# Kernel optimization log

Hardware: AMD Instinct MI355X
Metric: run time of the kernel (lower is better)

The kernel has to match this reference:

```python
import jax, jax.numpy as jnp
import numpy as np

B, CIN, H, W = 4, 128, 128, 128
CH = CIN // 2          # channels after transpose conv (= 64)
COUT = 64
N2 = (B * 2 * H * 2 * W) // 2  # active sites of x2 (half of fine grid)


def setup_inputs() -> dict:
    key = jax.random.key(0)
    ks = jax.random.split(key, 8)
    n = lambda k, s, sc=1.0: jax.random.normal(k, s, jnp.float32) * sc
    return {
        "x1": n(ks[0], (B, CIN, H, W)),
        "x2_feat": n(ks[1], (N2, CH)),
        "w_up": n(ks[2], (CIN, CH, 2, 2), 0.05),   # torch ConvTranspose2d layout [in, out, kh, kw]
        "b_up": n(ks[3], (CH,), 0.05),
        "w1": n(ks[4], (CH, CH, 3, 3), 0.05),      # torch Conv2d layout [out, in, kh, kw]
        "b1": n(ks[5], (CH,), 0.05),
        "a1": jnp.full((1,), 0.25, jnp.float32),   # nn.PReLU default init
        "w2": n(ks[6], (COUT, CH, 3, 3), 0.05),
        "b2": n(ks[7], (COUT,), 0.05),
        "a2": jnp.full((1,), 0.25, jnp.float32),
    }


def _prelu(x, a):
    return jnp.where(x >= 0, x, a * x)


def _conv3(x, w, b):
    y = jax.lax.conv_general_dilated(x, w, (1, 1), 'SAME',
                                     dimension_numbers=('NCHW', 'OIHW', 'NCHW'))
    return y + b[None, :, None, None]


def reference(x1, x2_feat, w_up, b_up, w1, b1, a1, w2, b2, a2):
    Bn, _, Hn, Wn = x1.shape
    # ConvTranspose2d k=2, s=2 (non-overlapping) as an einsum:
    # up[b,o,2i+p,2j+q] = sum_c x1[b,c,i,j] * w_up[c,o,p,q]
    up = jnp.einsum('bchw,copq->bohpwq', x1, w_up).reshape(Bn, CH, 2 * Hn, 2 * Wn)
    up = up + b_up[None, :, None, None]
    # addspvec: larger tensor keeps its indices; first len(b) feature rows
    # are overwritten by the smaller tensor's features (spconv raster order).
    f = jnp.transpose(up, (0, 2, 3, 1)).reshape(-1, CH)  # [B*2H*2W, CH]
    f = f.at[:x2_feat.shape[0]].set(x2_feat)
    merged = jnp.transpose(f.reshape(Bn, 2 * Hn, 2 * Wn, CH), (0, 3, 1, 2))
    # DoubleConv: (SparseConv2d 3x3 pad1 -> PReLU) x 2 (dense-equivalent)
    h = _prelu(_conv3(merged, w1, b1), a1[0])
    out = _prelu(_conv3(h, w2, b2), a2[0])
    return out
```

## Files before the change

kernel.cpp:

```cpp
#include <hip/hip_runtime.h>

typedef __attribute__((ext_vector_type(8))) short short8;
typedef __attribute__((ext_vector_type(4))) float f32x4;

#define HF 256
#define WF 256

typedef const __attribute__((address_space(1))) void gbl_void;
typedef __attribute__((address_space(3))) void lds_void;

__device__ __forceinline__ ushort f2bf(float f) {
    uint u = __builtin_bit_cast(uint, f);
    u = (u + 0x7FFFu + ((u >> 16) & 1u)) >> 16;
    return (ushort)u;
}
__device__ __forceinline__ uint pack2(float a, float b) {
    return (uint)f2bf(a) | ((uint)f2bf(b) << 16);
}
__device__ __forceinline__ float prelu(float v, float al) { return v >= 0.f ? v : al * v; }

__global__ __launch_bounds__(256) void k_wprep(const float* __restrict__ w1,
                                               const float* __restrict__ w2,
                                               const float* __restrict__ wup,
                                               ushort* __restrict__ wT1,
                                               ushort* __restrict__ wT2,
                                               ushort* __restrict__ wupT,
                                               uint4* __restrict__ zeroBuf) {
    int idx = blockIdx.x * 256 + threadIdx.x;
    if (blockIdx.x == 0 && threadIdx.x < 16)
        zeroBuf[threadIdx.x] = make_uint4(0u, 0u, 0u, 0u);
    if (idx < 36864) {
        int tap = idx >> 12;
        int oc  = idx & 4095;
        int src = oc * 9 + tap;
        wT1[idx] = f2bf(w1[src]);
        wT2[idx] = f2bf(w2[src]);
    }
    if (idx < 32768) {
        int out = idx >> 7;
        int c   = idx & 127;
        int k   = out >> 6;
        int o   = out & 63;
        wupT[idx] = f2bf(wup[c * 256 + o * 4 + k]);
    }
}

__global__ __launch_bounds__(512) void k_upsample_mfma(const float* __restrict__ x1,
                                                       const ushort* __restrict__ wupT,
                                                       const float* __restrict__ bup,
                                                       ushort* __restrict__ upB) {
    __shared__ __align__(16) char lds[81920];

    const int t   = threadIdx.x;
    const int l   = t & 63;
    const int l15 = l & 15;
    const int l4  = l >> 4;
    const int w   = t >> 6;
    const int pg  = w & 3;
    const int oh  = w >> 2;
    const int i   = blockIdx.x >> 1;
    const int j0  = (blockIdx.x & 1) * 64;
    const int z   = blockIdx.y;
    const int gb  = 2 + z;

    {
        const int j  = t & 63;
        const int cg = t >> 6;
        const size_t base = ((size_t)gb * 128) * 16384 + (size_t)i * 128 + j0 + j;
        float xv[16];
#pragma unroll
        for (int r = 0; r < 2; ++r)
#pragma unroll
            for (int cc = 0; cc < 8; ++cc)
                xv[r * 8 + cc] = x1[base + (size_t)(cg * 16 + r * 8 + cc) * 16384];
#pragma unroll
        for (int r = 0; r < 2; ++r) {
            short8 pk;
#pragma unroll
            for (int cc = 0; cc < 8; ++cc) pk[cc] = (short)f2bf(xv[r * 8 + cc]);
            int ad = (j * 256 + (cg * 16 + r * 8) * 2) ^ ((j & 15) << 4);
            *(short8*)(lds + ad) = pk;
        }
    }
    {
        const uint4* src = (const uint4*)wupT;
#pragma unroll
        for (int rep = 0; rep < 8; ++rep) {
            int q   = rep * 512 + t;
            int out = q >> 4, c16 = q & 15;
            int ad  = 16384 + ((out * 256 + c16 * 16) ^ ((out & 15) << 4));
            *(uint4*)(lds + ad) = src[q];
        }
    }
    float bvv[4];
#pragma unroll
    for (int ob = 0; ob < 4; ++ob) bvv[ob] = bup[ob * 16 + l15];
    __syncthreads();

    f32x4 acc[2][4];
#pragma unroll
    for (int kk = 0; kk < 2; ++kk)
#pragma unroll
        for (int ob = 0; ob < 4; ++ob) acc[kk][ob] = (f32x4){0.f, 0.f, 0.f, 0.f};

#pragma unroll
    for (int ks = 0; ks < 4; ++ks) {
        const int cb = ks * 64 + (l4 << 4);
        const int rowA = pg * 16 + l15;
        short8 xfr = *(const short8*)(lds + ((rowA * 256 + cb) ^ ((rowA & 15) << 4)));
#pragma unroll
        for (int kk = 0; kk < 2; ++kk)
#pragma unroll
            for (int ob = 0; ob < 4; ++ob) {
                int out = (oh * 2 + kk) * 64 + ob * 16 + l15;
                short8 wfr = *(const short8*)(lds + 16384 +
                              ((out * 256 + cb) ^ ((out & 15) << 4)));
                acc[kk][ob] = __builtin_amdgcn_mfma_f32_16x16x32_bf16(xfr, wfr, acc[kk][ob], 0, 0, 0);
            }
    }
    __syncthreads();

    ushort* OUT = (ushort*)lds;
#pragma unroll
    for (int kk = 0; kk < 2; ++kk) {
        const int k = oh * 2 + kk, p = k >> 1, q = k & 1;
#pragma unroll
        for (int ob = 0; ob < 4; ++ob) {
            const int o = ob * 16 + l15;
#pragma unroll
            for (int r = 0; r < 4; ++r) {
                int jl = pg * 16 + l4 * 4 + r;
                int x  = 2 * jl + q;
                OUT[(p * 128 + x) * 64 + o] = f2bf(acc[kk][ob][r] + bvv[ob]);
            }
        }
    }
    __syncthreads();

#pragma unroll
    for (int rep = 0; rep < 4; ++rep) {
        int idx = rep * 512 + t;
        int p   = idx >> 10;
        int y   = 2 * i + p;
        uint4 v = *(const uint4*)(lds + idx * 16);
        size_t g = (size_t)(z * HF + y) * 2048 + (size_t)j0 * 16 + (idx & 1023);
        ((uint4*)upB)[g] = v;
    }
}

template<int IN_MODE, int OUT_NHWC>
__global__ __launch_bounds__(1024, 1) void k_conv(const float* __restrict__ x2,
                                                  const ushort* __restrict__ upB,
                                                  const ushort* __restrict__ inB,
                                                  const ushort* __restrict__ wT,
                                                  const float* __restrict__ bias,
                                                  const float* __restrict__ alpha,
                                                  const uint4* __restrict__ zeroBuf,
                                                  ushort* __restrict__ outB,
                                                  float* __restrict__ outF) {
    __shared__ __align__(16) ushort inL[5120 * 8];
    __shared__ __align__(16) ushort wL[9 * 64 * 64];

    const int t   = threadIdx.x;
    const int wv  = t >> 6;
    const int l   = t & 63;
    const int l15 = l & 15;
    const int l4  = l >> 4;
    const int x0  = (blockIdx.x & 7) * 32;
    const int y0  = (blockIdx.x >> 3) * 16;
    const int b   = blockIdx.y;

    {
        const char* wTb = (const char*)wT;
#pragma unroll
        for (int rep = 0; rep < 4; ++rep) {
            int d   = rep * 1024 + t;
            int tap = d >> 9;
            int dp  = d & 511;
            int s   = (tap << 9) + (dp ^ ((dp >> 3) & 7));
            __builtin_amdgcn_global_load_lds(
                (gbl_void*)(wTb + (size_t)s * 16),
                (lds_void*)((char*)wL + (size_t)((rep << 10) + (wv << 6)) * 16),
                16, 0, 0);
        }
        if (wv < 8) {
            int d   = 4096 + (wv << 6) + l;
            int tap = d >> 9;
            int dp  = d & 511;
            int s   = (tap << 9) + (dp ^ ((dp >> 3) & 7));
            __builtin_amdgcn_global_load_lds(
                (gbl_void*)(wTb + (size_t)s * 16),
                (lds_void*)((char*)wL + (size_t)(4096 + (wv << 6)) * 16),
                16, 0, 0);
        }
    }

    if (IN_MODE == 1 || b >= 2) {
        const ushort* src0 = (IN_MODE == 1) ? inB : upB;
        const int bb = (IN_MODE == 1) ? b : (b - 2);
#pragma unroll
        for (int rep = 0; rep < 5; ++rep) {
            int d  = rep * 1024 + t;
            int r  = d / 272;
            int wi = d - r * 272;
            int wq = wi ^ ((wi >> 3) & 7);
            int x  = wq >> 3, c8 = wq & 7;
            int gy = y0 - 1 + r;
            int gx = x0 - 1 + x;
            const void* g;
            if (d < 4896 && (unsigned)gy < HF && (unsigned)gx < WF) {
                size_t pos = (size_t)(bb * HF + gy) * WF + gx;
                g = (const void*)(src0 + pos * 64 + c8 * 8);
            } else {
                g = (const void*)zeroBuf;
            }
            __builtin_amdgcn_global_load_lds(
                (gbl_void*)g,
                (lds_void*)((char*)inL + (size_t)((rep << 10) + (wv << 6)) * 16),
                16, 0, 0);
        }
    } else {
        for (int q = t; q < 18 * 34 * 8; q += 1024) {
            int r   = q / 272;
            int rem = q - r * 272;
            int x   = rem >> 3;
            int c8  = rem & 7;
            int gy = y0 - 1 + r;
            int gx = x0 - 1 + x;
            uint4 v = make_uint4(0u, 0u, 0u, 0u);
            if ((unsigned)gy < HF && (unsigned)gx < WF) {
                size_t pos = (size_t)(b * HF + gy) * WF + gx;
                const float4* s = (const float4*)(x2 + pos * 64 + c8 * 8);
                float4 u0 = s[0], u1 = s[1];
                v = make_uint4(pack2(u0.x, u0.y), pack2(u0.z, u0.w),
                               pack2(u1.x, u1.y), pack2(u1.z, u1.w));
            }
            int ad = (q * 16) ^ ((x & 7) << 4);
            *(uint4*)((char*)inL + ad) = v;
        }
    }
    __syncthreads();

    f32x4 acc[2][4];
#pragma unroll
    for (int m = 0; m < 2; ++m)
#pragma unroll
        for (int nf = 0; nf < 4; ++nf) acc[m][nf] = (f32x4){0.f, 0.f, 0.f, 0.f};

#pragma unroll
    for (int tap = 0; tap < 9; ++tap) {
        const int ky = tap / 3;
        const int kx = tap % 3;
        const char* wPage = (const char*)wL + tap * 8192;
#pragma unroll
        for (int ks = 0; ks < 2; ++ks) {
            short8 wfr[4];
#pragma unroll
            for (int nf = 0; nf < 4; ++nf) {
                int o = nf * 16 + l15;
                int ad = (o * 128 + ks * 64 + (l4 << 4)) ^ ((o & 7) << 4);
                wfr[nf] = *(const short8*)(wPage + ad);
            }
#pragma unroll
            for (int m = 0; m < 2; ++m) {
                int ry = wv + ky;
                int xl = m * 16 + l15 + kx;
                int ad = ((ry * 34 + xl) * 128 + ks * 64 + (l4 << 4)) ^ ((xl & 7) << 4);
                short8 ifr = *(const short8*)((const char*)inL + ad);
#pragma unroll
                for (int nf = 0; nf < 4; ++nf) {
                    if (OUT_NHWC)
                        acc[m][nf] = __builtin_amdgcn_mfma_f32_16x16x32_bf16(
                            wfr[nf], ifr, acc[m][nf], 0, 0, 0);
                    else
                        acc[m][nf] = __builtin_amdgcn_mfma_f32_16x16x32_bf16(
                            ifr, wfr[nf], acc[m][nf], 0, 0, 0);
                }
            }
        }
    }

    const float al = alpha[0];
    const int y = y0 + wv;
    if (OUT_NHWC) {
        float4 bv[4];
#pragma unroll
        for (int nf = 0; nf < 4; ++nf) bv[nf] = *(const float4*)(bias + nf * 16 + (l4 << 2));
#pragma unroll
        for (int m = 0; m < 2; ++m) {
            int x = x0 + m * 16 + l15;
#pragma unroll
            for (int nf = 0; nf < 4; ++nf) {
                f32x4 v = acc[m][nf];
                uint lo = pack2(prelu(v.x + bv[nf].x, al), prelu(v.y + bv[nf].y, al));
                uint hi = pack2(prelu(v.z + bv[nf].z, al), prelu(v.w + bv[nf].w, al));
                int cb = nf * 16 + (l4 << 2);
                *(uint2*)(outB + ((size_t)(b * HF + y) * WF + x) * 64 + cb) = make_uint2(lo, hi);
            }
        }
    } else {
        float bb[4];
#pragma unroll
        for (int nf = 0; nf < 4; ++nf) bb[nf] = bias[nf * 16 + l15];
#pragma unroll
        for (int m = 0; m < 2; ++m) {
            int xb = x0 + m * 16 + (l4 << 2);
#pragma unroll
            for (int nf = 0; nf < 4; ++nf) {
                f32x4 v = acc[m][nf];
                int cout = nf * 16 + l15;
                float4 st;
                st.x = prelu(v.x + bb[nf], al);
                st.y = prelu(v.y + bb[nf], al);
                st.z = prelu(v.z + bb[nf], al);
                st.w = prelu(v.w + bb[nf], al);
                *(float4*)(outF + (((size_t)b * 64 + cout) << 16) + y * WF + xb) = st;
            }
        }
    }
}

extern "C" void kernel_launch(void* const* d_in, const int* in_sizes, int n_in,
                              void* d_out, int out_size, void* d_ws, size_t ws_size,
                              hipStream_t stream) {
    const float* x1  = (const float*)d_in[0];
    const float* x2  = (const float*)d_in[1];
    const float* wup = (const float*)d_in[2];
    const float* bup = (const float*)d_in[3];
    const float* w1  = (const float*)d_in[4];
    const float* b1  = (const float*)d_in[5];
    const float* a1  = (const float*)d_in[6];
    const float* w2  = (const float*)d_in[7];
    const float* b2  = (const float*)d_in[8];
    const float* a2  = (const float*)d_in[9];

    char* ws = (char*)d_ws;
    ushort* upB  = (ushort*)ws;
    ushort* hB   = (ushort*)(ws + (size_t)(16 << 20));
    ushort* wT1  = (ushort*)(ws + (size_t)(48 << 20));
    ushort* wT2  = wT1 + 9 * 64 * 64;
    ushort* wupT = wT2 + 9 * 64 * 64;
    uint4*  zeroBuf = (uint4*)(ws + (size_t)(49 << 20));
    float* out = (float*)d_out;

    k_wprep<<<144, 256, 0, stream>>>(w1, w2, wup, wT1, wT2, wupT, zeroBuf);
    k_upsample_mfma<<<dim3(256, 2), 512, 0, stream>>>(x1, wupT, bup, upB);
    k_conv<0, 1><<<dim3(128, 4), 1024, 0, stream>>>(x2, upB, nullptr, wT1, b1, a1, zeroBuf, hB, nullptr);
    k_conv<1, 0><<<dim3(128, 4), 1024, 0, stream>>>(nullptr, nullptr, hB, wT2, b2, a2, zeroBuf, nullptr, out);
}
```

Measured before the change: 80.78 us.

## Halve conv tile height and stream weights in tap chunks for two blocks/CU

```diff
diff --git a/kernel.cpp b/kernel.cpp
--- a/kernel.cpp
+++ b/kernel.cpp
@@ -149,17 +149,17 @@
 }
 
 template<int IN_MODE, int OUT_NHWC>
-__global__ __launch_bounds__(1024, 1) void k_conv(const float* __restrict__ x2,
-                                                  const ushort* __restrict__ upB,
-                                                  const ushort* __restrict__ inB,
-                                                  const ushort* __restrict__ wT,
-                                                  const float* __restrict__ bias,
-                                                  const float* __restrict__ alpha,
-                                                  const uint4* __restrict__ zeroBuf,
-                                                  ushort* __restrict__ outB,
-                                                  float* __restrict__ outF) {
-    __shared__ __align__(16) ushort inL[5120 * 8];
-    __shared__ __align__(16) ushort wL[9 * 64 * 64];
+__global__ __launch_bounds__(512, 2) void k_conv(const float* __restrict__ x2,
+                                                 const ushort* __restrict__ upB,
+                                                 const ushort* __restrict__ inB,
+                                                 const ushort* __restrict__ wT,
+                                                 const float* __restrict__ bias,
+                                                 const float* __restrict__ alpha,
+                                                 const uint4* __restrict__ zeroBuf,
+                                                 ushort* __restrict__ outB,
+                                                 float* __restrict__ outF) {
+    __shared__ __align__(16) ushort inL[2816 * 8];
+    __shared__ __align__(16) ushort wL[4 * 64 * 64];
 
     const int t   = threadIdx.x;
     const int wv  = t >> 6;
@@ -167,60 +167,54 @@
     const int l15 = l & 15;
     const int l4  = l >> 4;
     const int x0  = (blockIdx.x & 7) * 32;
-    const int y0  = (blockIdx.x >> 3) * 16;
+    const int y0  = (blockIdx.x >> 3) * 8;
     const int b   = blockIdx.y;
 
-    {
-        const char* wTb = (const char*)wT;
-#pragma unroll
-        for (int rep = 0; rep < 4; ++rep) {
-            int d   = rep * 1024 + t;
-            int tap = d >> 9;
+    const char* wTb = (const char*)wT;
+
+    auto stage_w = [&](int s) {
+        const int nrep = (s == 2) ? 1 : 4;
+        for (int rep = 0; rep < nrep; ++rep) {
+            int d   = rep * 512 + t;
+            int tl  = d >> 9;
             int dp  = d & 511;
-            int s   = (tap << 9) + (dp ^ ((dp >> 3) & 7));
+            int st  = s * 4 + tl;
+            int srcq = (st << 9) + (dp ^ ((dp >> 3) & 7));
             __builtin_amdgcn_global_load_lds(
-                (gbl_void*)(wTb + (size_t)s * 16),
-                (lds_void*)((char*)wL + (size_t)((rep << 10) + (wv << 6)) * 16),
+                (gbl_void*)(wTb + (size_t)srcq * 16),
+                (lds_void*)((char*)wL + (size_t)((rep << 9) + (wv << 6)) * 16),
                 16, 0, 0);
         }
-        if (wv < 8) {
-            int d   = 4096 + (wv << 6) + l;
-            int tap = d >> 9;
-            int dp  = d & 511;
-            int s   = (tap << 9) + (dp ^ ((dp >> 3) & 7));
-            __builtin_amdgcn_global_load_lds(
-                (gbl_void*)(wTb + (size_t)s * 16),
-                (lds_void*)((char*)wL + (size_t)(4096 + (wv << 6)) * 16),
-                16, 0, 0);
-        }
-    }
+    };
 
     if (IN_MODE == 1 || b >= 2) {
         const ushort* src0 = (IN_MODE == 1) ? inB : upB;
         const int bb = (IN_MODE == 1) ? b : (b - 2);
 #pragma unroll
-        for (int rep = 0; rep < 5; ++rep) {
-            int d  = rep * 1024 + t;
-            int r  = d / 272;
-            int wi = d - r * 272;
-            int wq = wi ^ ((wi >> 3) & 7);
-            int x  = wq >> 3, c8 = wq & 7;
-            int gy = y0 - 1 + r;
-            int gx = x0 - 1 + x;
-            const void* g;
-            if (d < 4896 && (unsigned)gy < HF && (unsigned)gx < WF) {
-                size_t pos = (size_t)(bb * HF + gy) * WF + gx;
-                g = (const void*)(src0 + pos * 64 + c8 * 8);
-            } else {
-                g = (const void*)zeroBuf;
-            }
-            __builtin_amdgcn_global_load_lds(
-                (gbl_void*)g,
-                (lds_void*)((char*)inL + (size_t)((rep << 10) + (wv << 6)) * 16),
-                16, 0, 0);
+        for (int rep = 0; rep < 6; ++rep) {
+            int d = rep * 512 + t;
+            if (d < 2720) {
+                int r  = d / 272;
+                int wi = d - r * 272;
+                int wq = wi ^ ((wi >> 3) & 7);
+                int x  = wq >> 3, c8 = wq & 7;
+                int gy = y0 - 1 + r;
+                int gx = x0 - 1 + x;
+                const void* g;
+                if ((unsigned)gy < HF && (unsigned)gx < WF) {
+                    size_t pos = (size_t)(bb * HF + gy) * WF + gx;
+                    g = (const void*)(src0 + pos * 64 + c8 * 8);
+                } else {
+                    g = (const void*)zeroBuf;
+                }
+                __builtin_amdgcn_global_load_lds(
+                    (gbl_void*)g,
+                    (lds_void*)((char*)inL + (size_t)((rep << 9) + (wv << 6)) * 16),
+                    16, 0, 0);
+            }
         }
     } else {
-        for (int q = t; q < 18 * 34 * 8; q += 1024) {
+        for (int q = t; q < 2720; q += 512) {
             int r   = q / 272;
             int rem = q - r * 272;
             int x   = rem >> 3;
@@ -239,6 +233,7 @@
             *(uint4*)((char*)inL + ad) = v;
         }
     }
+    stage_w(0);
     __syncthreads();
 
     f32x4 acc[2][4];
@@ -247,38 +242,52 @@
 #pragma unroll
         for (int nf = 0; nf < 4; ++nf) acc[m][nf] = (f32x4){0.f, 0.f, 0.f, 0.f};
 
-#pragma unroll
-    for (int tap = 0; tap < 9; ++tap) {
-        const int ky = tap / 3;
-        const int kx = tap % 3;
-        const char* wPage = (const char*)wL + tap * 8192;
-#pragma unroll
-        for (int ks = 0; ks < 2; ++ks) {
-            short8 wfr[4];
-#pragma unroll
-            for (int nf = 0; nf < 4; ++nf) {
-                int o = nf * 16 + l15;
-                int ad = (o * 128 + ks * 64 + (l4 << 4)) ^ ((o & 7) << 4);
-                wfr[nf] = *(const short8*)(wPage + ad);
-            }
-#pragma unroll
-            for (int m = 0; m < 2; ++m) {
-                int ry = wv + ky;
-                int xl = m * 16 + l15 + kx;
-                int ad = ((ry * 34 + xl) * 128 + ks * 64 + (l4 << 4)) ^ ((xl & 7) << 4);
-                short8 ifr = *(const short8*)((const char*)inL + ad);
+    auto k_chunk = [&](int base, int ntaps) {
+#pragma unroll
+        for (int tl = 0; tl < 4; ++tl) {
+            if (tl >= ntaps) break;
+            const int tap = base + tl;
+            const int ky = tap / 3;
+            const int kx = tap % 3;
+            const char* wPage = (const char*)wL + tl * 8192;
+#pragma unroll
+            for (int ks = 0; ks < 2; ++ks) {
+                short8 wfr[4];
 #pragma unroll
                 for (int nf = 0; nf < 4; ++nf) {
-                    if (OUT_NHWC)
-                        acc[m][nf] = __builtin_amdgcn_mfma_f32_16x16x32_bf16(
-                            wfr[nf], ifr, acc[m][nf], 0, 0, 0);
-                    else
-                        acc[m][nf] = __builtin_amdgcn_mfma_f32_16x16x32_bf16(
-                            ifr, wfr[nf], acc[m][nf], 0, 0, 0);
+                    int o = nf * 16 + l15;
+                    int ad = (o * 128 + ks * 64 + (l4 << 4)) ^ ((o & 7) << 4);
+                    wfr[nf] = *(const short8*)(wPage + ad);
                 }
-            }
-        }
-    }
+#pragma unroll
+                for (int m = 0; m < 2; ++m) {
+                    int ry = wv + ky;
+                    int xl = m * 16 + l15 + kx;
+                    int ad = ((ry * 34 + xl) * 128 + ks * 64 + (l4 << 4)) ^ ((xl & 7) << 4);
+                    short8 ifr = *(const short8*)((const char*)inL + ad);
+#pragma unroll
+                    for (int nf = 0; nf < 4; ++nf) {
+                        if (OUT_NHWC)
+                            acc[m][nf] = __builtin_amdgcn_mfma_f32_16x16x32_bf16(
+                                wfr[nf], ifr, acc[m][nf], 0, 0, 0);
+                        else
+                            acc[m][nf] = __builtin_amdgcn_mfma_f32_16x16x32_bf16(
+                                ifr, wfr[nf], acc[m][nf], 0, 0, 0);
+                    }
+                }
+            }
+        }
+    };
+
+    k_chunk(0, 4);
+    __syncthreads();
+    stage_w(1);
+    __syncthreads();
+    k_chunk(4, 4);
+    __syncthreads();
+    stage_w(2);
+    __syncthreads();
+    k_chunk(8, 1);
 
     const float al = alpha[0];
     const int y = y0 + wv;
@@ -345,6 +354,6 @@
 
     k_wprep<<<144, 256, 0, stream>>>(w1, w2, wup, wT1, wT2, wupT, zeroBuf);
     k_upsample_mfma<<<dim3(256, 2), 512, 0, stream>>>(x1, wupT, bup, upB);
-    k_conv<0, 1><<<dim3(128, 4), 1024, 0, stream>>>(x2, upB, nullptr, wT1, b1, a1, zeroBuf, hB, nullptr);
-    k_conv<1, 0><<<dim3(128, 4), 1024, 0, stream>>>(nullptr, nullptr, hB, wT2, b2, a2, zeroBuf, nullptr, out);
-}
+    k_conv<0, 1><<<dim3(256, 4), 512, 0, stream>>>(x2, upB, nullptr, wT1, b1, a1, zeroBuf, hB, nullptr);
+    k_conv<1, 0><<<dim3(256, 4), 512, 0, stream>>>(nullptr, nullptr, hB, wT2, b2, a2, zeroBuf, nullptr, out);
+}
```

Result: no change. 82.12 us (+1.7%).
